# Kernel optimization log

Hardware: AMD Instinct MI355X
Metric: run time of the kernel (lower is better)

## Reference

```python
import jax, jax.numpy as jnp
import numpy as np

DIM, NWIN, TOPK, HEADS = 128, 8, 4, 4
SCALE = DIM ** -0.5


def conv2d(x, w, groups=1, pad=0):
    return jax.lax.conv_general_dilated(
        x, w, (1, 1), [(pad, pad), (pad, pad)],
        feature_group_count=groups,
        dimension_numbers=('NCHW', 'OIHW', 'NCHW'))


def to_windows(elem):
    # elem: [b, C, H, W] -> [b, n_hw, hs, ws, C]
    b, c, h, w = elem.shape
    hs, ws = h // NWIN, w // NWIN
    y = elem.transpose(0, 2, 3, 1)                       # b H W C
    y = y.reshape(b, NWIN, hs, NWIN, ws, c)
    y = y.transpose(0, 1, 3, 2, 4, 5)                    # b n_h n_w hs ws C
    return y.reshape(b, NWIN * NWIN, hs, ws, c)


def from_windows(out, hs, ws):
    # out: [b, n_hw, s_hw, C] -> [b, H, W, C]
    b, nw, s, c = out.shape
    y = out.reshape(b, NWIN, NWIN, hs, ws, c)
    y = y.transpose(0, 1, 3, 2, 4, 5)
    return y.reshape(b, NWIN * hs, NWIN * ws, c)


def window_attention(elem, mlp_w, mlp_b):
    # elem: [b, 3*dim, H, W]
    b, c3, h, w = elem.shape
    hs, ws = h // NWIN, w // NWIN
    win = to_windows(elem)                               # b n_hw hs ws 3C
    q = win[..., :DIM]                                   # b n_hw hs ws C
    kv = win[..., DIM:]                                  # b n_hw hs ws 2C
    nw, s = NWIN * NWIN, hs * ws
    q_pix = q.reshape(b, nw, s, DIM)
    kv_pix = kv.reshape(b, nw, s, 2 * DIM)
    # window-level 'max' projection (WinProj)
    q_win = jax.lax.stop_gradient(q_pix.max(axis=2))             # b nw C
    k_win = jax.lax.stop_gradient(kv_pix[..., :DIM].max(axis=2))  # b nw C
    # top-k routing (diff_routing=False, mul_weight='none' -> only indices used)
    logits = jnp.einsum('bic,bjc->bij', q_win * SCALE, k_win)    # b nw nw
    _, r_idx = jax.lax.top_k(logits, TOPK)                       # b nw topk
    # gather selected kv windows: b nw topk s 2C
    kv_sel = jax.vmap(lambda kvb, ib: kvb[ib])(kv_pix, r_idx)
    kv_sel = kv_sel.reshape(b, nw, TOPK * s, 2 * DIM)
    k_sel = kv_sel[..., :DIM].reshape(b, nw, TOPK * s, HEADS, DIM // HEADS)
    v_sel = kv_sel[..., DIM:].reshape(b, nw, TOPK * s, HEADS, DIM // HEADS)
    qh = q_pix.reshape(b, nw, s, HEADS, DIM // HEADS)
    attn = jnp.einsum('bwshd,bwthd->bwhst', qh * SCALE, k_sel)
    attn = jax.nn.softmax(attn, axis=-1)
    out = jnp.einsum('bwhst,bwthd->bwshd', attn, v_sel)
    out = out.reshape(b, nw, s, DIM)
    out = from_windows(out, hs, ws)                      # b H W C
    out = jnp.einsum('bhwi,oi->bhwo', out, mlp_w) + mlp_b
    return out.transpose(0, 3, 1, 2)                     # b C H W


def setup_inputs() -> dict:
    key = jax.random.key(0)
    ks = jax.random.split(key, 12)
    d = DIM
    return {
        'x': jax.random.normal(ks[0], (1, d, 128, 128), jnp.float32),
        'qkv2_w': jax.random.normal(ks[1], (3 * d, d, 1, 1), jnp.float32) * 0.05,
        'dw3_w': jax.random.normal(ks[2], (3 * d, 1, 3, 3), jnp.float32) * 0.1,
        'pw3_w': jax.random.normal(ks[3], (3 * d, (3 * d) // (3 * HEADS), 1, 1), jnp.float32) * 0.05,
        'dw5_w': jax.random.normal(ks[4], (3 * d, 1, 5, 5), jnp.float32) * 0.1,
        'pw5_w': jax.random.normal(ks[5], (3 * d, (3 * d) // (3 * HEADS), 1, 1), jnp.float32) * 0.05,
        'mlp_w': jax.random.normal(ks[6], (d, d), jnp.float32) * 0.05,
        'mlp_b': jnp.zeros((d,), jnp.float32),
        'proj_w': jax.random.normal(ks[7], (d, 3 * d, 1, 1), jnp.float32) * 0.05,
        'ln_g': jnp.ones((d,), jnp.float32),
        'ln_b': jnp.zeros((d,), jnp.float32),
    }


def reference(x, qkv2_w, dw3_w, pw3_w, dw5_w, pw5_w, mlp_w, mlp_b, proj_w, ln_g, ln_b):
    qkv = conv2d(x, qkv2_w)                              # b 3C H W
    branches = [qkv]
    for dw, pw, k in ((dw3_w, pw3_w, 3), (dw5_w, pw5_w, 5)):
        y = conv2d(qkv, dw, groups=3 * DIM, pad=k // 2)  # depthwise
        y = conv2d(y, pw, groups=3 * HEADS)              # grouped 1x1
        branches.append(y)
    outs = [window_attention(e, mlp_w, mlp_b) for e in branches]
    out = jnp.concatenate(outs, axis=1)                  # b 3C H W
    out = conv2d(out, proj_w)                            # b C H W
    # ln2d: LayerNorm over channel dim
    mu = out.mean(axis=1, keepdims=True)
    var = out.var(axis=1, keepdims=True)
    out = (out - mu) * jax.lax.rsqrt(var + 1e-5)
    out = out * ln_g[None, :, None, None] + ln_b[None, :, None, None]
    return out
```

## Files before the change

### kernel.cpp

```cpp
#include <hip/hip_runtime.h>
#include <math.h>

#define P 16384
#define SCALEF 0.08838834764831845f
#define QSCALE 0.12752075616290145f

typedef short bf16x8 __attribute__((ext_vector_type(8)));
typedef float f32x4 __attribute__((ext_vector_type(4)));

__device__ __forceinline__ unsigned short f2bf(float x) {
  union { float f; unsigned int u; } v; v.f = x;
  unsigned int r = v.u + 0x7fffu + ((v.u >> 16) & 1u);
  return (unsigned short)(r >> 16);
}
__device__ __forceinline__ unsigned int packbf(float a, float b) {
  return (unsigned int)f2bf(a) | ((unsigned int)f2bf(b) << 16);
}
__device__ __forceinline__ unsigned int pr2(float a, float b) {
  union { float f; unsigned int u; } ua, ub; ua.f = a; ub.f = b;
  return __builtin_amdgcn_perm(ub.u + 0x8000u, ua.u + 0x8000u, 0x07060302u);
}
__device__ __forceinline__ unsigned int pk2(float a, float b) {
  unsigned int r;
  asm("v_cvt_pk_bf16_f32 %0, %1, %2" : "=v"(r) : "v"(a), "v"(b));
  return r;
}
#define EXP2F(x) __builtin_amdgcn_exp2f(x)

template<int NS, int JT>
__global__ __launch_bounds__(256) void k_conv_mfma(
    const float* __restrict__ in, const float* __restrict__ w,
    const float* __restrict__ bias, float* __restrict__ out,
    const int IC, const int in_zstr, const int out_zstr)
{
  const int p0  = blockIdx.x * (JT * 64);
  const int oc0 = blockIdx.y * 64;
  in  += (size_t)blockIdx.z * (size_t)in_zstr;
  out += (size_t)blockIdx.z * (size_t)out_zstr;
  const int tid = threadIdx.x;
  const int wv = tid >> 6;
  const int lane = tid & 63;
  const int qi = lane & 15, g = lane >> 4;

  __shared__ __align__(16) unsigned int bS[NS][JT * 64 * 16];
  __shared__ __align__(16) unsigned int aS[NS][64 * 16];

  const f32x4 fz = {0.f, 0.f, 0.f, 0.f};
  f32x4 acc[JT][4];
  #pragma unroll
  for (int j = 0; j < JT; ++j)
    #pragma unroll
    for (int o = 0; o < 4; ++o) acc[j][o] = fz;

  for (int k0 = 0; k0 < IC; k0 += 32) {
    __syncthreads();
    {
      const int kB = tid >> 4;
      const int pB = (tid & 15) * (JT * 4);
      const float* r0 = in + (size_t)(k0 + 2 * kB) * P + p0 + pB;
      #pragma unroll
      for (int half = 0; half < JT / 2; ++half) {
        float x0[8], x1[8];
        #pragma unroll
        for (int v = 0; v < 2; ++v) {
          float4 a = ((const float4*)r0)[half * 2 + v];
          float4 c = ((const float4*)(r0 + P))[half * 2 + v];
          x0[4*v] = a.x; x0[4*v+1] = a.y; x0[4*v+2] = a.z; x0[4*v+3] = a.w;
          x1[4*v] = c.x; x1[4*v+1] = c.y; x1[4*v+2] = c.z; x1[4*v+3] = c.w;
        }
        #pragma unroll
        for (int ii = 0; ii < 8; ++ii) {
          const int i8 = (ii + tid) & 7;
          const int i = half * 8 + i8;
          const unsigned idx = (unsigned)((pB + i) * 16 + (kB ^ ((i & 3) << 2)));
          const unsigned u0 = __float_as_uint(x0[i8]);
          const unsigned u1 = __float_as_uint(x1[i8]);
          bS[0][idx] = __builtin_amdgcn_perm(u1, u0, 0x07060302u);
          const float r0f = x0[i8] - __uint_as_float(u0 & 0xffff0000u);
          const float r1f = x1[i8] - __uint_as_float(u1 & 0xffff0000u);
          bS[1][idx] = pr2(r0f, r1f);
        }
      }
    }
    {
      const int oA = tid >> 2;
      const int kA = (tid & 3) * 8;
      const float* rw = w + (size_t)(oc0 + oA) * IC + k0 + kA;
      float4 wa = ((const float4*)rw)[0];
      float4 wb = ((const float4*)rw)[1];
      float y[8] = {wa.x, wa.y, wa.z, wa.w, wb.x, wb.y, wb.z, wb.w};
      #pragma unroll
      for (int i = 0; i < 4; ++i) {
        const int dd = (kA >> 1) + i;
        const unsigned idx = (unsigned)(oA * 16 + (dd ^ ((oA & 3) << 2)));
        const unsigned u0 = __float_as_uint(y[2*i]);
        const unsigned u1 = __float_as_uint(y[2*i+1]);
        aS[0][idx] = __builtin_amdgcn_perm(u1, u0, 0x07060302u);
        const float r0f = y[2*i]   - __uint_as_float(u0 & 0xffff0000u);
        const float r1f = y[2*i+1] - __uint_as_float(u1 & 0xffff0000u);
        aS[1][idx] = pr2(r0f, r1f);
      }
    }
    __syncthreads();

    bf16x8 aF[4][NS];
    #pragma unroll
    for (int o = 0; o < 4; ++o) {
      const unsigned ab = (unsigned)((o * 16 + qi) * 16 + 4 * (g ^ (qi & 3)));
      #pragma unroll
      for (int s = 0; s < NS; ++s)
        aF[o][s] = *(const bf16x8*)&aS[s][ab];
    }
    #pragma unroll
    for (int j = 0; j < JT; ++j) {
      const unsigned bb = (unsigned)(((wv * JT + j) * 16 + qi) * 16 + 4 * (g ^ (qi & 3)));
      const bf16x8 b0 = *(const bf16x8*)&bS[0][bb];
      const bf16x8 b1 = *(const bf16x8*)&bS[1][bb];
      #pragma unroll
      for (int o = 0; o < 4; ++o) {
        acc[j][o] = __builtin_amdgcn_mfma_f32_16x16x32_bf16(aF[o][0], b0, acc[j][o], 0, 0, 0);
        acc[j][o] = __builtin_amdgcn_mfma_f32_16x16x32_bf16(aF[o][0], b1, acc[j][o], 0, 0, 0);
        acc[j][o] = __builtin_amdgcn_mfma_f32_16x16x32_bf16(aF[o][1], b0, acc[j][o], 0, 0, 0);
      }
    }
  }

  float bv[4][4];
  #pragma unroll
  for (int o = 0; o < 4; ++o)
    #pragma unroll
    for (int t = 0; t < 4; ++t)
      bv[o][t] = bias ? bias[oc0 + o * 16 + 4 * g + t] : 0.f;

  #pragma unroll
  for (int j = 0; j < JT; ++j) {
    const int px = p0 + (wv * JT + j) * 16 + qi;
    #pragma unroll
    for (int o = 0; o < 4; ++o)
      #pragma unroll
      for (int t = 0; t < 4; ++t)
        out[(size_t)(oc0 + o * 16 + 4 * g + t) * P + px] = acc[j][o][t] + bv[o][t];
  }
}

__global__ __launch_bounds__(128) void k_foldw(
    const float* __restrict__ proj_w, const float* __restrict__ mlp_w,
    float* __restrict__ Wc)
{
  const int o = blockIdx.x;
  const int b = blockIdx.y;
  const int i = threadIdx.x;
  const float* pw = proj_w + o * 384 + b * 128;
  float acc = 0.f;
  for (int j = 0; j < 128; ++j)
    acc += pw[j] * mlp_w[j * 128 + i];
  Wc[o * 384 + b * 128 + i] = acc;
}
__global__ __launch_bounds__(128) void k_foldb(
    const float* __restrict__ proj_w, const float* __restrict__ mlp_b,
    float* __restrict__ bc)
{
  const int o = threadIdx.x;
  float acc = 0.f;
  for (int c = 0; c < 384; ++c) acc += proj_w[o * 384 + c] * mlp_b[c & 127];
  bc[o] = acc;
}

__global__ __launch_bounds__(256) void k_dwf(
    const float* __restrict__ in, const float* __restrict__ w3,
    const float* __restrict__ w5, float* __restrict__ out3,
    float* __restrict__ out5)
{
  const int c  = blockIdx.y;
  const int ty = blockIdx.x;
  const int y0 = ty * 16;
  __shared__ float tS[20][136];
  const float* ip = in + (size_t)c * P;

  if (threadIdx.x < 20) {
    tS[threadIdx.x][0] = 0.f; tS[threadIdx.x][1] = 0.f;
    tS[threadIdx.x][130] = 0.f; tS[threadIdx.x][131] = 0.f;
  }
  for (int e = threadIdx.x; e < 640; e += 256) {
    const int r = e >> 5, q = e & 31;
    const int gy = y0 + r - 2;
    float4 v = make_float4(0.f, 0.f, 0.f, 0.f);
    if (gy >= 0 && gy < 128) v = *(const float4*)&ip[gy * 128 + q * 4];
    *(float4*)&tS[r][2 + q * 4] = v;
  }
  __syncthreads();

  float a3[9], a5[25];
  #pragma unroll
  for (int i = 0; i < 9; ++i)  a3[i] = w3[c * 9 + i];
  #pragma unroll
  for (int i = 0; i < 25; ++i) a5[i] = w5[c * 25 + i];

  const int py  = threadIdx.x >> 4;
  const int px0 = (threadIdx.x & 15) * 8;
  float o3[8] = {}, o5[8] = {};
  #pragma unroll
  for (int r = 0; r < 5; ++r) {
    float4 sa = *(const float4*)&tS[py + r][px0];
    float4 sb = *(const float4*)&tS[py + r][px0 + 4];
    float4 sc = *(const float4*)&tS[py + r][px0 + 8];
    const float s[12] = {sa.x, sa.y, sa.z, sa.w, sb.x, sb.y, sb.z, sb.w,
                         sc.x, sc.y, sc.z, sc.w};
    #pragma unroll
    for (int j = 0; j < 8; ++j) {
      float acc = a5[r * 5 + 0] * s[j];
      #pragma unroll
      for (int d = 1; d < 5; ++d) acc += a5[r * 5 + d] * s[j + d];
      o5[j] += acc;
    }
    if (r >= 1 && r <= 3) {
      #pragma unroll
      for (int j = 0; j < 8; ++j) {
        float b = a3[(r - 1) * 3 + 0] * s[j + 1];
        b += a3[(r - 1) * 3 + 1] * s[j + 2];
        b += a3[(r - 1) * 3 + 2] * s[j + 3];
        o3[j] += b;
      }
    }
  }
  const size_t ob = (size_t)c * P + (y0 + py) * 128 + px0;
  float4* p3 = (float4*)&out3[ob];
  float4* p5 = (float4*)&out5[ob];
  p3[0] = make_float4(o3[0], o3[1], o3[2], o3[3]);
  p3[1] = make_float4(o3[4], o3[5], o3[6], o3[7]);
  p5[0] = make_float4(o5[0], o5[1], o5[2], o5[3]);
  p5[1] = make_float4(o5[4], o5[5], o5[6], o5[7]);
}

__global__ __launch_bounds__(256) void k_pw2(
    const float* in0, const float* __restrict__ w0, float* out0,
    const float* in1, const float* __restrict__ w1, float* out1)
{
  const float* in = blockIdx.z ? in1 : in0;
  const float* w  = blockIdx.z ? w1 : w0;
  float*      out = blockIdx.z ? out1 : out0;
  const int g = blockIdx.y;
  const int p = blockIdx.x * 256 + threadIdx.x;
  __shared__ float wL[1024];
  for (int e = threadIdx.x; e < 1024; e += 256) wL[e] = w[g * 1024 + e];
  __syncthreads();
  float r[32];
  #pragma unroll
  for (int i = 0; i < 32; ++i) r[i] = in[(g * 32 + i) * P + p];
  #pragma unroll
  for (int o = 0; o < 32; ++o) {
    float acc = 0.f;
    #pragma unroll
    for (int i = 0; i < 32; ++i) acc += wL[o * 32 + i] * r[i];
    out[(g * 32 + o) * P + p] = acc;
  }
}

__global__ __launch_bounds__(256) void k_winmax(
    const float* __restrict__ e0, const float* __restrict__ e1,
    const float* __restrict__ e2, float* __restrict__ qwin,
    float* __restrict__ kwin)
{
  const int b = blockIdx.y;
  const int wIdx = blockIdx.x;
  const float* e = (b == 0) ? e0 : ((b == 1) ? e1 : e2);
  const int wy = wIdx >> 3, wx = wIdx & 7;
  const int wv = threadIdx.x >> 6;
  const int lane = threadIdx.x & 63;
  const int half = lane >> 5, sub = lane & 31;
  const int row = sub >> 1, px8 = (sub & 1) * 8;
  const int base_off = (wy * 16 + row) * 128 + wx * 16 + px8;

  #pragma unroll 4
  for (int it = 0; it < 32; ++it) {
    const int c = it * 8 + wv * 2 + half;
    const float4* p4 = (const float4*)&e[(size_t)c * P + base_off];
    float4 v0 = p4[0], v1 = p4[1];
    float m = fmaxf(fmaxf(fmaxf(v0.x, v0.y), fmaxf(v0.z, v0.w)),
                    fmaxf(fmaxf(v1.x, v1.y), fmaxf(v1.z, v1.w)));
    #pragma unroll
    for (int s = 1; s <= 16; s <<= 1)
      m = fmaxf(m, __shfl_xor(m, s, 64));
    if (sub == 0) {
      if (c < 128) qwin[(b * 64 + wIdx) * 128 + c] = m;
      else         kwin[(b * 64 + wIdx) * 128 + (c - 128)] = m;
    }
  }
}

__global__ __launch_bounds__(256) void k_topk(
    const float* __restrict__ qwin, const float* __restrict__ kwin,
    int* __restrict__ ridx)
{
  const int b = blockIdx.y;
  const int i = blockIdx.x * 4 + (threadIdx.x >> 6);
  const int j = threadIdx.x & 63;
  const float4* q4 = (const float4*)&qwin[(b * 64 + i) * 128];
  const float4* k4 = (const float4*)&kwin[(b * 64 + j) * 128];
  float v = 0.f;
  #pragma unroll
  for (int t = 0; t < 32; ++t) {
    float4 a = q4[t], c = k4[t];
    v += a.x * c.x + a.y * c.y + a.z * c.z + a.w * c.w;
  }
  int res[4];
  #pragma unroll
  for (int r = 0; r < 4; ++r) {
    float bv = v; int bj = j;
    #pragma unroll
    for (int s = 1; s < 64; s <<= 1) {
      const float ov = __shfl_xor(bv, s, 64);
      const int   oj = __shfl_xor(bj, s, 64);
      if (ov > bv || (ov == bv && oj < bj)) { bv = ov; bj = oj; }
    }
    res[r] = bj;
    if (j == bj) v = -INFINITY;
  }
  if (j == 0)
    *(int4*)&ridx[(b * 64 + i) * 4] = make_int4(res[0], res[1], res[2], res[3]);
}

__global__ __launch_bounds__(256) void k_repack(
    const float* __restrict__ e0, const float* __restrict__ e1,
    const float* __restrict__ e2, unsigned int* __restrict__ kvimg,
    unsigned int* __restrict__ qimg)
{
  const int fl = blockIdx.x + 64 * (blockIdx.y + 4 * blockIdx.z);
  const int nf = (fl & 7) * 96 + (fl >> 3);
  const int w = nf & 63, h = (nf >> 6) & 3, b = nf >> 8;
  const float* e = (b == 0) ? e0 : ((b == 1) ? e1 : e2);
  const int wy = w >> 3, wx = w & 7;
  const int jbase = wy * 16 * 128 + wx * 16;
  const int t = threadIdx.x;
  unsigned int* kwin_img = kvimg + (size_t)((b * 4 + h) * 64 + w) * 8192;
  unsigned int* qwin_img = qimg  + (size_t)((b * 4 + h) * 64 + w) * 4096;

  {
    const int key = t;
    const int hw = jbase + (key >> 4) * 128 + (key & 15);
    const float* eK = e + (size_t)(128 + h * 32) * P + hw;
    const float* eQ = e + (size_t)(h * 32) * P + hw;
    const int half = key >> 7, kl = key & 127;
    unsigned int* kd = kwin_img + half * 4096 + kl * 16;
    unsigned int* qd = qwin_img + key * 16;
    #pragma unroll
    for (int dd = 0; dd < 16; ++dd) {
      float k0 = eK[(size_t)(2 * dd) * P], k1 = eK[(size_t)(2 * dd + 1) * P];
      kd[dd ^ ((kl & 3) << 2)] = packbf(k0, k1);
      float q0 = eQ[(size_t)(2 * dd) * P] * QSCALE;
      float q1 = eQ[(size_t)(2 * dd + 1) * P] * QSCALE;
      qd[dd] = packbf(q0, q1);
    }
  }
  {
    const int half = t >> 7, tt = t & 127;
    const int d = tt >> 2;
    const int kp0 = (tt & 3) * 16;
    const float* eV = e + (size_t)(256 + h * 32 + d) * P;
    unsigned int* vd = kwin_img + half * 4096 + 2048 + d * 64;
    #pragma unroll
    for (int i = 0; i < 16; ++i) {
      const int kp2 = kp0 + i;
      const int key = half * 128 + kp2 * 2;
      const int hw = jbase + (key >> 4) * 128 + (key & 15);
      float v0 = eV[hw], v1 = eV[hw + 1];
      vd[kp2 ^ ((d & 7) << 2)] = packbf(v0, v1);
    }
  }
}

__global__ __launch_bounds__(512, 4) void k_attn_mfma(
    const unsigned int* __restrict__ kvimg, const unsigned int* __restrict__ qimg,
    const int* __restrict__ ridx, float* __restrict__ attnch)
{
  const int fl = blockIdx.x + 64 * (blockIdx.y + 4 * blockIdx.z);
  const int nf = (fl & 7) * 96 + (fl >> 3);
  const int w = nf & 63, h = (nf >> 6) & 3, b = nf >> 8;
  const int tid = threadIdx.x;
  const int wv = tid >> 6, lane = tid & 63;
  const int qi = lane & 15, g = lane >> 4;
  const int wy = w >> 3, wx = w & 7;

  __shared__ __align__(16) unsigned int kvbuf[2][4096];

  const unsigned int* kwin = kvimg + (size_t)((b * 4 + h) * 64) * 8192;
  const unsigned int* qwin = qimg + (size_t)((b * 4 + h) * 64 + w) * 4096;

  bf16x8 qv[2];
  #pragma unroll
  for (int s = 0; s < 2; ++s) {
    union { uint4 u; bf16x8 v; } tq;
    tq.u = *(const uint4*)(qwin + ((wv * 2 + s) * 16 + qi) * 16 + g * 4);
    qv[s] = tq.v;
  }
  const int4 jv = *(const int4*)(ridx + (b * 64 + w) * 4);
  const int ja[4] = {jv.x, jv.y, jv.z, jv.w};

  const f32x4 fz = {0.f, 0.f, 0.f, 0.f};
  float m[2], l[2];
  f32x4 acc[2][2];
  #pragma unroll
  for (int s = 0; s < 2; ++s) {
    m[s] = -3.0e38f; l[s] = 0.f; acc[s][0] = fz; acc[s][1] = fz;
  }

  uint4 st0, st1;
  {
    const uint4* s4 = (const uint4*)(kwin + (size_t)ja[0] * 8192);
    st0 = s4[tid]; st1 = s4[512 + tid];
  }

#define SOFTMAX_PACK(SC, S, PB) {                                           \
    float wmax = -3.0e38f;                                                  \
    _Pragma("unroll") for (int c = 0; c < 4; ++c)                           \
      _Pragma("unroll") for (int u = 0; u < 2; ++u)                         \
        _Pragma("unroll") for (int t2 = 0; t2 < 4; ++t2)                    \
          wmax = fmaxf(wmax, SC[c][u][t2]);                                 \
    wmax = fmaxf(wmax, __shfl_xor(wmax, 16, 64));                           \
    wmax = fmaxf(wmax, __shfl_xor(wmax, 32, 64));                           \
    const float mnew = fmaxf(m[S], wmax);                                   \
    const float corr = EXP2F(m[S] - mnew);                                  \
    m[S] = mnew;                                                            \
    acc[S][0] *= corr; acc[S][1] *= corr;                                   \
    float psum = 0.f;                                                       \
    _Pragma("unroll") for (int c = 0; c < 4; ++c)                           \
      _Pragma("unroll") for (int u = 0; u < 2; ++u) {                       \
        const float p0 = EXP2F(SC[c][u][0] - mnew);                         \
        const float p1 = EXP2F(SC[c][u][1] - mnew);                         \
        const float p2 = EXP2F(SC[c][u][2] - mnew);                         \
        const float p3 = EXP2F(SC[c][u][3] - mnew);                         \
        psum += (p0 + p1) + (p2 + p3);                                      \
        PB[c][2 * u]     = pk2(p0, p1);                                     \
        PB[c][2 * u + 1] = pk2(p2, p3);                                     \
      }                                                                     \
    l[S] = l[S] * corr + psum;                                              \
  }

  for (int ch = 0; ch < 8; ++ch) {
    {
      uint4* d4 = (uint4*)kvbuf[ch & 1];
      d4[tid] = st0; d4[512 + tid] = st1;
    }
    if (ch < 7) {
      const int nx = ch + 1;
      const uint4* s4 = (const uint4*)(kwin + (size_t)ja[nx >> 1] * 8192
                                       + (size_t)(nx & 1) * 4096);
      st0 = s4[tid]; st1 = s4[512 + tid];
    }
    __syncthreads();

    const unsigned int* bc = kvbuf[ch & 1];
    const bf16x8* kp = (const bf16x8*)bc;
    const unsigned short* vsh = (const unsigned short*)(bc + 2048);

    f32x4 scA[4][2], scB[4][2];
    __builtin_amdgcn_s_setprio(1);
    #pragma unroll
    for (int c = 0; c < 4; ++c) {
      #pragma unroll
      for (int u = 0; u < 2; ++u) {
        const int key = 32 * c + 8 * (qi >> 2) + 4 * u + (qi & 3);
        const bf16x8 ka = kp[key * 4 + (g ^ (qi & 3))];
        scA[c][u] = __builtin_amdgcn_mfma_f32_16x16x32_bf16(ka, qv[0], fz, 0, 0, 0);
        scB[c][u] = __builtin_amdgcn_mfma_f32_16x16x32_bf16(ka, qv[1], fz, 0, 0, 0);
      }
    }
    __builtin_amdgcn_s_setprio(0);
    unsigned int pbA[4][4], pbB[4][4];
    SOFTMAX_PACK(scA, 0, pbA);
    SOFTMAX_PACK(scB, 1, pbB);
    __builtin_amdgcn_s_setprio(1);
    #pragma unroll
    for (int c = 0; c < 4; ++c) {
      #pragma unroll
      for (int dt = 0; dt < 2; ++dt) {
        const int d0 = dt * 16 + qi;
        const bf16x8 va = *(const bf16x8*)&vsh[
            (unsigned)((d0 * 128 + 32 * c + 8 * g) ^ ((d0 & 7) << 3))];
        union { unsigned int u4[4]; bf16x8 v; } pva, pvb;
        pva.u4[0] = pbA[c][0]; pva.u4[1] = pbA[c][1];
        pva.u4[2] = pbA[c][2]; pva.u4[3] = pbA[c][3];
        pvb.u4[0] = pbB[c][0]; pvb.u4[1] = pbB[c][1];
        pvb.u4[2] = pbB[c][2]; pvb.u4[3] = pbB[c][3];
        acc[0][dt] = __builtin_amdgcn_mfma_f32_16x16x32_bf16(va, pva.v, acc[0][dt], 0, 0, 0);
        acc[1][dt] = __builtin_amdgcn_mfma_f32_16x16x32_bf16(va, pvb.v, acc[1][dt], 0, 0, 0);
      }
    }
    __builtin_amdgcn_s_setprio(0);
  }
#undef SOFTMAX_PACK

  #pragma unroll
  for (int s = 0; s < 2; ++s) {
    float lsum = l[s];
    lsum += __shfl_xor(lsum, 16, 64);
    lsum += __shfl_xor(lsum, 32, 64);
    const float inv = 1.f / lsum;
    const int hwq = (wy * 16 + wv * 2 + s) * 128 + wx * 16 + qi;
    #pragma unroll
    for (int dt = 0; dt < 2; ++dt)
      #pragma unroll
      for (int t = 0; t < 4; ++t) {
        const int d = dt * 16 + 4 * g + t;
        attnch[(size_t)(b * 128 + h * 32 + d) * P + hwq] = acc[s][dt][t] * inv;
      }
  }
}

__global__ __launch_bounds__(256) void k_ln(
    const float* __restrict__ in, const float* __restrict__ gg,
    const float* __restrict__ bta, float* __restrict__ out)
{
  const int l = threadIdx.x & 63;
  const int grp = threadIdx.x >> 6;
  const int p = blockIdx.x * 64 + l;
  __shared__ float s1[4][64], s2[4][64];
  float vals[32];
  float a = 0.f, b2 = 0.f;
  #pragma unroll
  for (int i = 0; i < 32; ++i) {
    float v = in[(size_t)(grp * 32 + i) * P + p];
    vals[i] = v; a += v; b2 += v * v;
  }
  s1[grp][l] = a; s2[grp][l] = b2;
  __syncthreads();
  const float sum = s1[0][l] + s1[1][l] + s1[2][l] + s1[3][l];
  const float sq  = s2[0][l] + s2[1][l] + s2[2][l] + s2[3][l];
  const float mu = sum * (1.f / 128.f);
  const float var = sq * (1.f / 128.f) - mu * mu;
  const float rs = rsqrtf(var + 1e-5f);
  #pragma unroll
  for (int i = 0; i < 32; ++i) {
    const int c = grp * 32 + i;
    out[(size_t)c * P + p] = (vals[i] - mu) * rs * gg[c] + bta[c];
  }
}

extern "C" void kernel_launch(void* const* d_in, const int* in_sizes, int n_in,
                              void* d_out, int out_size, void* d_ws, size_t ws_size,
                              hipStream_t stream)
{
  (void)in_sizes; (void)n_in; (void)out_size;
  const float* x      = (const float*)d_in[0];
  const float* qkv2_w = (const float*)d_in[1];
  const float* dw3_w  = (const float*)d_in[2];
  const float* pw3_w  = (const float*)d_in[3];
  const float* dw5_w  = (const float*)d_in[4];
  const float* pw5_w  = (const float*)d_in[5];
  const float* mlp_w  = (const float*)d_in[6];
  const float* mlp_b  = (const float*)d_in[7];
  const float* proj_w = (const float*)d_in[8];
  const float* ln_g   = (const float*)d_in[9];
  const float* ln_b   = (const float*)d_in[10];

  float* ws = (float*)d_ws;
  const size_t CH = (size_t)384 * P;
  float* qkv    = ws;
  float* dwt3   = ws + CH;
  float* y3     = ws + 2 * CH;
  float* y5     = ws + 3 * CH;
  float* qwin   = ws + 5 * CH;
  float* kwin   = qwin + 3 * 64 * 128;
  int*   ridx   = (int*)(kwin + 3 * 64 * 128);
  float* Wc     = (float*)(ridx + 768);
  float* bc     = Wc + 128 * 384;
  unsigned int* kvimg = (unsigned int*)(ws + 4 * CH);
  unsigned int* qimg  = (unsigned int*)dwt3;
  float* attnch = y3;
  float* projo  = qkv;
  (void)ws_size;

  k_foldw<<<dim3(128, 3), 128, 0, stream>>>(proj_w, mlp_w, Wc);
  k_foldb<<<1, 128, 0, stream>>>(proj_w, mlp_b, bc);

  k_conv_mfma<2, 2><<<dim3(128, 6, 1), 256, 0, stream>>>(x, qkv2_w, nullptr, qkv, 128, 0, 0);
  k_dwf<<<dim3(8, 384), 256, 0, stream>>>(qkv, dw3_w, dw5_w, dwt3, y5);
  k_pw2<<<dim3(64, 12, 2), 256, 0, stream>>>(dwt3, pw3_w, y3, y5, pw5_w, y5);
  k_winmax<<<dim3(64, 3), 256, 0, stream>>>(qkv, y3, y5, qwin, kwin);
  k_topk<<<dim3(16, 3), 256, 0, stream>>>(qwin, kwin, ridx);
  k_repack<<<dim3(64, 4, 3), 256, 0, stream>>>(qkv, y3, y5, kvimg, qimg);
  k_attn_mfma<<<dim3(64, 4, 3), 512, 0, stream>>>(kvimg, qimg, ridx, attnch);
  k_conv_mfma<2, 2><<<dim3(128, 2, 1), 256, 0, stream>>>(attnch, Wc, bc, projo, 384, 0, 0);
  k_ln<<<dim3(256), 256, 0, stream>>>(projo, ln_g, ln_b, (float*)d_out);
}
```

Baseline: 216.5 us.

## Fuse projection conv with LayerNorm and add lazy softmax max rescaling

Replaces the separate projection conv and LayerNorm kernels with one kernel. It computes all 128 output channels for a 64-pixel tile using split-bf16 MFMA (three products to approximate fp32), then applies LayerNorm in registers. This removes the projection output round-trip through global memory and one launch. Separately, the online softmax in attention now skips the max update and accumulator rescale unless some lane's new max exceeds the running max by more than 8 (in log2 units). That saves exp and multiply work, at the cost of exponentials up to 2^8 that could matter for fp32 or bf16 range.

```diff
diff --git a/kernel.cpp b/kernel.cpp
--- a/kernel.cpp
+++ b/kernel.cpp
@@ -143,6 +143,108 @@
   }
 }
 
+__global__ __launch_bounds__(256) void k_projln(
+    const float* __restrict__ in, const float* __restrict__ w,
+    const float* __restrict__ bias, const float* __restrict__ ln_g,
+    const float* __restrict__ ln_b, float* __restrict__ out)
+{
+  const int p0 = blockIdx.x * 64;
+  const int tid = threadIdx.x;
+  const int wv = tid >> 6;
+  const int lane = tid & 63;
+  const int qi = lane & 15, g = lane >> 4;
+
+  __shared__ __align__(16) unsigned int bS[2][64 * 16];
+  __shared__ __align__(16) unsigned int aS[2][128 * 16];
+
+  const f32x4 fz = {0.f, 0.f, 0.f, 0.f};
+  f32x4 acc[8];
+  #pragma unroll
+  for (int o = 0; o < 8; ++o) acc[o] = fz;
+
+  for (int k0 = 0; k0 < 384; k0 += 32) {
+    __syncthreads();
+    {
+      const int kB = tid >> 4;
+      const int pB = (tid & 15) * 4;
+      const float* r0 = in + (size_t)(k0 + 2 * kB) * P + p0 + pB;
+      float4 a = *(const float4*)r0;
+      float4 c = *(const float4*)(r0 + P);
+      const float x0[4] = {a.x, a.y, a.z, a.w};
+      const float x1[4] = {c.x, c.y, c.z, c.w};
+      #pragma unroll
+      for (int i = 0; i < 4; ++i) {
+        const unsigned idx = (unsigned)((pB + i) * 16 + (kB ^ (i << 2)));
+        const unsigned u0 = __float_as_uint(x0[i]);
+        const unsigned u1 = __float_as_uint(x1[i]);
+        bS[0][idx] = __builtin_amdgcn_perm(u1, u0, 0x07060302u);
+        const float r0f = x0[i] - __uint_as_float(u0 & 0xffff0000u);
+        const float r1f = x1[i] - __uint_as_float(u1 & 0xffff0000u);
+        bS[1][idx] = pr2(r0f, r1f);
+      }
+    }
+    {
+      const int oA = tid >> 1;
+      const int kA = (tid & 1) * 16;
+      const float* rw = w + (size_t)oA * 384 + k0 + kA;
+      float4 wa = ((const float4*)rw)[0];
+      float4 wb = ((const float4*)rw)[1];
+      float4 wc = ((const float4*)rw)[2];
+      float4 wd = ((const float4*)rw)[3];
+      const float y[16] = {wa.x, wa.y, wa.z, wa.w, wb.x, wb.y, wb.z, wb.w,
+                           wc.x, wc.y, wc.z, wc.w, wd.x, wd.y, wd.z, wd.w};
+      #pragma unroll
+      for (int i = 0; i < 8; ++i) {
+        const int dd = (kA >> 1) + i;
+        const unsigned idx = (unsigned)(oA * 16 + (dd ^ ((oA & 3) << 2)));
+        const unsigned u0 = __float_as_uint(y[2*i]);
+        const unsigned u1 = __float_as_uint(y[2*i+1]);
+        aS[0][idx] = __builtin_amdgcn_perm(u1, u0, 0x07060302u);
+        const float r0f = y[2*i]   - __uint_as_float(u0 & 0xffff0000u);
+        const float r1f = y[2*i+1] - __uint_as_float(u1 & 0xffff0000u);
+        aS[1][idx] = pr2(r0f, r1f);
+      }
+    }
+    __syncthreads();
+
+    const unsigned bb = (unsigned)((wv * 16 + qi) * 16 + 4 * (g ^ (qi & 3)));
+    const bf16x8 b0 = *(const bf16x8*)&bS[0][bb];
+    const bf16x8 b1 = *(const bf16x8*)&bS[1][bb];
+    #pragma unroll
+    for (int o = 0; o < 8; ++o) {
+      const unsigned ab = (unsigned)((o * 16 + qi) * 16 + 4 * (g ^ (qi & 3)));
+      const bf16x8 a0 = *(const bf16x8*)&aS[0][ab];
+      const bf16x8 a1 = *(const bf16x8*)&aS[1][ab];
+      acc[o] = __builtin_amdgcn_mfma_f32_16x16x32_bf16(a0, b0, acc[o], 0, 0, 0);
+      acc[o] = __builtin_amdgcn_mfma_f32_16x16x32_bf16(a0, b1, acc[o], 0, 0, 0);
+      acc[o] = __builtin_amdgcn_mfma_f32_16x16x32_bf16(a1, b0, acc[o], 0, 0, 0);
+    }
+  }
+
+  const int px = p0 + wv * 16 + qi;
+  float vch[8][4];
+  float sum = 0.f, sq = 0.f;
+  #pragma unroll
+  for (int o = 0; o < 8; ++o)
+    #pragma unroll
+    for (int t = 0; t < 4; ++t) {
+      const float v = acc[o][t] + bias[o * 16 + 4 * g + t];
+      vch[o][t] = v; sum += v; sq += v * v;
+    }
+  sum += __shfl_xor(sum, 16, 64); sum += __shfl_xor(sum, 32, 64);
+  sq  += __shfl_xor(sq, 16, 64);  sq  += __shfl_xor(sq, 32, 64);
+  const float mu = sum * (1.f / 128.f);
+  const float var = sq * (1.f / 128.f) - mu * mu;
+  const float rs = rsqrtf(var + 1e-5f);
+  #pragma unroll
+  for (int o = 0; o < 8; ++o)
+    #pragma unroll
+    for (int t = 0; t < 4; ++t) {
+      const int oc = o * 16 + 4 * g + t;
+      out[(size_t)oc * P + px] = (vch[o][t] - mu) * rs * ln_g[oc] + ln_b[oc];
+    }
+}
+
 __global__ __launch_bounds__(128) void k_foldw(
     const float* __restrict__ proj_w, const float* __restrict__ mlp_w,
     float* __restrict__ Wc)
@@ -418,17 +520,20 @@
           wmax = fmaxf(wmax, SC[c][u][t2]);                                 \
     wmax = fmaxf(wmax, __shfl_xor(wmax, 16, 64));                           \
     wmax = fmaxf(wmax, __shfl_xor(wmax, 32, 64));                           \
-    const float mnew = fmaxf(m[S], wmax);                                   \
-    const float corr = EXP2F(m[S] - mnew);                                  \
-    m[S] = mnew;                                                            \
-    acc[S][0] *= corr; acc[S][1] *= corr;                                   \
+    float corr = 1.f;                                                       \
+    if (!__all(wmax - m[S] <= 8.f)) {                    \
+      const float mnew = fmaxf(m[S], wmax);                                 \
+      corr = EXP2F(m[S] - mnew);                                            \
+      m[S] = mnew;                                                          \
+      acc[S][0] *= corr; acc[S][1] *= corr;                                 \
+    }                                                                       \
     float psum = 0.f;                                                       \
     _Pragma("unroll") for (int c = 0; c < 4; ++c)                           \
       _Pragma("unroll") for (int u = 0; u < 2; ++u) {                       \
-        const float p0 = EXP2F(SC[c][u][0] - mnew);                         \
-        const float p1 = EXP2F(SC[c][u][1] - mnew);                         \
-        const float p2 = EXP2F(SC[c][u][2] - mnew);                         \
-        const float p3 = EXP2F(SC[c][u][3] - mnew);                         \
+        const float p0 = EXP2F(SC[c][u][0] - m[S]);                         \
+        const float p1 = EXP2F(SC[c][u][1] - m[S]);                         \
+        const float p2 = EXP2F(SC[c][u][2] - m[S]);                         \
+        const float p3 = EXP2F(SC[c][u][3] - m[S]);                         \
         psum += (p0 + p1) + (p2 + p3);                                      \
         PB[c][2 * u]     = pk2(p0, p1);                                     \
         PB[c][2 * u + 1] = pk2(p2, p3);                                     \
@@ -504,35 +609,6 @@
         const int d = dt * 16 + 4 * g + t;
         attnch[(size_t)(b * 128 + h * 32 + d) * P + hwq] = acc[s][dt][t] * inv;
       }
-  }
-}
-
-__global__ __launch_bounds__(256) void k_ln(
-    const float* __restrict__ in, const float* __restrict__ gg,
-    const float* __restrict__ bta, float* __restrict__ out)
-{
-  const int l = threadIdx.x & 63;
-  const int grp = threadIdx.x >> 6;
-  const int p = blockIdx.x * 64 + l;
-  __shared__ float s1[4][64], s2[4][64];
-  float vals[32];
-  float a = 0.f, b2 = 0.f;
-  #pragma unroll
-  for (int i = 0; i < 32; ++i) {
-    float v = in[(size_t)(grp * 32 + i) * P + p];
-    vals[i] = v; a += v; b2 += v * v;
-  }
-  s1[grp][l] = a; s2[grp][l] = b2;
-  __syncthreads();
-  const float sum = s1[0][l] + s1[1][l] + s1[2][l] + s1[3][l];
-  const float sq  = s2[0][l] + s2[1][l] + s2[2][l] + s2[3][l];
-  const float mu = sum * (1.f / 128.f);
-  const float var = sq * (1.f / 128.f) - mu * mu;
-  const float rs = rsqrtf(var + 1e-5f);
-  #pragma unroll
-  for (int i = 0; i < 32; ++i) {
-    const int c = grp * 32 + i;
-    out[(size_t)c * P + p] = (vals[i] - mu) * rs * gg[c] + bta[c];
   }
 }
 
@@ -567,7 +643,6 @@
   unsigned int* kvimg = (unsigned int*)(ws + 4 * CH);
   unsigned int* qimg  = (unsigned int*)dwt3;
   float* attnch = y3;
-  float* projo  = qkv;
   (void)ws_size;
 
   k_foldw<<<dim3(128, 3), 128, 0, stream>>>(proj_w, mlp_w, Wc);
@@ -580,6 +655,5 @@
   k_topk<<<dim3(16, 3), 256, 0, stream>>>(qwin, kwin, ridx);
   k_repack<<<dim3(64, 4, 3), 256, 0, stream>>>(qkv, y3, y5, kvimg, qimg);
   k_attn_mfma<<<dim3(64, 4, 3), 512, 0, stream>>>(kvimg, qimg, ridx, attnch);
-  k_conv_mfma<2, 2><<<dim3(128, 2, 1), 256, 0, stream>>>(attnch, Wc, bc, projo, 384, 0, 0);
-  k_ln<<<dim3(256), 256, 0, stream>>>(projo, ln_g, ln_b, (float*)d_out);
-}
+  k_projln<<<dim3(256), 256, 0, stream>>>(attnch, Wc, bc, ln_g, ln_b, (float*)d_out);
+}
```

Measured after the change: 217.4 us. About the same (+0.4%).
